# Kernel optimization log

Measured on AMD Instinct MI355X. Metric: run time of the kernel, lower is better.

## Reference

```python
import jax, jax.numpy as jnp
import numpy as np
import math

B, S, D, H = 2, 2048, 1024, 16
HD = D // H  # head_dims = 64


def setup_inputs() -> dict:
    key = jax.random.key(0)
    ks = jax.random.split(key, 8)
    sc = 1.0 / math.sqrt(D)
    return {
        "queries": jax.random.normal(ks[0], (B, S, D), jnp.float32),
        "keys":    jax.random.normal(ks[1], (B, S, D), jnp.float32),
        "values":  jax.random.normal(ks[2], (B, S, D), jnp.float32),
        # causal mask: 1 where attending allowed, 0 where blocked (masked_fill on ==0)
        "mask": jnp.tril(jnp.ones((S, S), jnp.int32)),
        "Wq": jax.random.normal(ks[3], (D, D), jnp.float32) * sc,
        "bq": jnp.zeros((D,), jnp.float32),
        "Wk": jax.random.normal(ks[4], (D, D), jnp.float32) * sc,
        "bk": jnp.zeros((D,), jnp.float32),
        "Wv": jax.random.normal(ks[5], (D, D), jnp.float32) * sc,
        "bv": jnp.zeros((D,), jnp.float32),
        "Wo": jax.random.normal(ks[6], (D, D), jnp.float32) * sc,
        "bo": jnp.zeros((D,), jnp.float32),
    }


def _split_heads(x):
    # (B, S, D) -> (B, H, S, HD)
    return x.reshape(B, S, H, HD).transpose(0, 2, 1, 3)


def reference(queries, keys, values, mask, Wq, bq, Wk, bk, Wv, bv, Wo, bo):
    q = queries @ Wq + bq
    k = keys @ Wk + bk
    # NOTE: faithful to source quirk — V is projected from the ALREADY-PROJECTED keys
    # (original: keys = self.W_keys(keys); values = self.W_values(keys))
    v = k @ Wv + bv
    q, k, v = _split_heads(q), _split_heads(k), _split_heads(v)
    # naive full NxN attention, as in the source
    scores = jnp.einsum("bhqd,bhkd->bhqk", q, k) / math.sqrt(HD)
    scores = jnp.where(mask == 0, jnp.float32(-1e9), scores)
    probs = jax.nn.softmax(scores, axis=-1)
    attn = jnp.einsum("bhqk,bhkd->bhqd", probs, v)
    attn = attn.transpose(0, 2, 1, 3).reshape(B, S, D)
    return attn @ Wo + bo
```

## Files before the change

kernel.cpp:

```cpp
#include <hip/hip_runtime.h>

typedef unsigned short u16;
typedef unsigned int u32;
typedef __bf16 bf16x8 __attribute__((ext_vector_type(8)));
typedef float f32x4 __attribute__((ext_vector_type(4)));
typedef float f32x16 __attribute__((ext_vector_type(16)));
typedef unsigned int u32x4v __attribute__((ext_vector_type(4)));

#define MFMA16(a, b, c) __builtin_amdgcn_mfma_f32_16x16x32_bf16(a, b, c, 0, 0, 0)
#define MFMA32(a, b, c) __builtin_amdgcn_mfma_f32_32x32x16_bf16(a, b, c, 0, 0, 0)

__device__ __forceinline__ void gload16(const void* g, void* l) {
  __builtin_amdgcn_global_load_lds((const __attribute__((address_space(1))) void*)g,
                                   (__attribute__((address_space(3))) void*)l, 16, 0, 0);
}

__device__ __forceinline__ u16 f2bf(float f) {
  u32 u = __builtin_bit_cast(u32, f);
  u += 0x7fffu + ((u >> 16) & 1u);
  return (u16)(u >> 16);
}
__device__ __forceinline__ u32 pack2(float a, float b) {
  u32 r;
  asm("v_cvt_pk_bf16_f32 %0, %1, %2" : "=v"(r) : "v"(a), "v"(b));
  return r;
}

__global__ __launch_bounds__(256) void cvt_kernel(const float* __restrict__ q,
                                                  const float* __restrict__ k,
                                                  u16* __restrict__ qb,
                                                  u16* __restrict__ kb) {
  const float* src = blockIdx.y ? k : q;
  u16* dst = blockIdx.y ? kb : qb;
  size_t i = (size_t)blockIdx.x * 256 + threadIdx.x;
  float4 v = ((const float4*)src)[i];
  uint2 o;
  o.x = pack2(v.x, v.y);
  o.y = pack2(v.z, v.w);
  ((uint2*)dst)[i] = o;
}

__global__ __launch_bounds__(256) void wtrans_kernel(const float* W0, const float* W1,
                                                     const float* W2, const float* W3,
                                                     u16* T0, u16* T1, u16* T2, u16* T3) {
  int z = blockIdx.z;
  const float* W = z == 0 ? W0 : z == 1 ? W1 : z == 2 ? W2 : W3;
  u16* T = z == 0 ? T0 : z == 1 ? T1 : z == 2 ? T2 : T3;
  __shared__ float tile[64][65];
  int tr = blockIdx.y * 64, tc = blockIdx.x * 64;
  int tid = threadIdx.x;
  int c4 = (tid & 15) * 4, r0 = tid >> 4;
#pragma unroll
  for (int i = 0; i < 4; i++) {
    int r = r0 + i * 16;
    float4 v = *(const float4*)(W + (size_t)(tr + r) * 1024 + tc + c4);
    tile[r][c4 + 0] = v.x; tile[r][c4 + 1] = v.y;
    tile[r][c4 + 2] = v.z; tile[r][c4 + 3] = v.w;
  }
  __syncthreads();
#pragma unroll
  for (int i = 0; i < 2; i++) {
    int c = tid + i * 256;
    int n = c >> 3, kg = c & 7;
    uint4 o;
    o.x = pack2(tile[kg * 8 + 0][n], tile[kg * 8 + 1][n]);
    o.y = pack2(tile[kg * 8 + 2][n], tile[kg * 8 + 3][n]);
    o.z = pack2(tile[kg * 8 + 4][n], tile[kg * 8 + 5][n]);
    o.w = pack2(tile[kg * 8 + 6][n], tile[kg * 8 + 7][n]);
    *(uint4*)(T + (size_t)(tc + n) * 1024 + tr + kg * 8) = o;
  }
}

template <int MODE>
__global__ __launch_bounds__(256) void gemm_kernel(
    const u16* A0, const u16* B0, const float* bias0, void* C0, float scale0,
    const u16* A1, const u16* B1, const float* bias1, void* C1, float scale1,
    int M, int N, int K) {
  const u16* A = A0; const u16* Bt = B0; const float* bias = bias0; void* Cout = C0;
  float scale = scale0;
  if (blockIdx.z) { A = A1; Bt = B1; bias = bias1; Cout = C1; scale = scale1; }

  __shared__ __attribute__((aligned(16))) char sAB[49152];
  const int tid = threadIdx.x, lane = tid & 63, w = tid >> 6;
  const int l15 = lane & 15, quad = lane >> 4;
  const int wm = (w >> 1) * 64, wn = (w & 1) * 32;
  const int m0 = blockIdx.y * 128, n0 = blockIdx.x * 64;

  const int lrow = lane >> 3, lcg = (lane & 7) ^ lrow;
  const u16* aP[4]; const u16* bP[2];
#pragma unroll
  for (int i = 0; i < 4; i++)
    aP[i] = A + (size_t)(m0 + w * 32 + i * 8 + lrow) * K + lcg * 8;
#pragma unroll
  for (int i = 0; i < 2; i++)
    bP[i] = Bt + (size_t)(n0 + w * 16 + i * 8 + lrow) * K + lcg * 8;

  int aoff[4], boff[2];
#pragma unroll
  for (int t = 0; t < 4; t++) {
    int ra = wm + t * 16 + l15;
    aoff[t] = ra * 128 + ((quad ^ (ra & 7)) * 16);
  }
#pragma unroll
  for (int t = 0; t < 2; t++) {
    int rb = wn + t * 16 + l15;
    boff[t] = 16384 + rb * 128 + ((quad ^ (rb & 7)) * 16);
  }

#pragma unroll
  for (int i = 0; i < 4; i++) { gload16(aP[i], sAB + w * 4096 + i * 1024); aP[i] += 64; }
#pragma unroll
  for (int i = 0; i < 2; i++) { gload16(bP[i], sAB + 16384 + w * 2048 + i * 1024); bP[i] += 64; }

  f32x4 acc[4][2] = {};
  int cur = 0;
  for (int k = 0; k < K; k += 64) {
    __syncthreads();
    if (k + 64 < K) {
      char* dst = sAB + (cur ^ 1) * 24576;
#pragma unroll
      for (int i = 0; i < 4; i++) { gload16(aP[i], dst + w * 4096 + i * 1024); aP[i] += 64; }
#pragma unroll
      for (int i = 0; i < 2; i++) { gload16(bP[i], dst + 16384 + w * 2048 + i * 1024); bP[i] += 64; }
    }
    const char* buf = sAB + cur * 24576;
#pragma unroll
    for (int kt = 0; kt < 2; kt++) {
      bf16x8 af[4], bfr[2];
#pragma unroll
      for (int t = 0; t < 4; t++) af[t] = *(const bf16x8*)(buf + (aoff[t] ^ (kt * 64)));
#pragma unroll
      for (int t = 0; t < 2; t++) bfr[t] = *(const bf16x8*)(buf + (boff[t] ^ (kt * 64)));
#pragma unroll
      for (int mt = 0; mt < 4; mt++)
#pragma unroll
        for (int nt = 0; nt < 2; nt++)
          acc[mt][nt] = MFMA16(af[mt], bfr[nt], acc[mt][nt]);
    }
    cur ^= 1;
  }

#pragma unroll
  for (int nt = 0; nt < 2; nt++) {
    int col = n0 + wn + nt * 16 + l15;
    float bv = bias[col];
#pragma unroll
    for (int mt = 0; mt < 4; mt++) {
      int row = m0 + wm + mt * 16 + quad * 4;
      if (MODE == 0) {
        u16* C = (u16*)Cout;
#pragma unroll
        for (int r = 0; r < 4; r++)
          C[(size_t)(row + r) * N + col] = f2bf((acc[mt][nt][r] + bv) * scale);
      } else if (MODE == 1) {
        u16* C = (u16*)Cout;
        int hh = col >> 6, hd = col & 63;
        int bb = row >> 11, s = row & 2047;
        uint2 o;
        o.x = pack2((acc[mt][nt][0] + bv) * scale, (acc[mt][nt][1] + bv) * scale);
        o.y = pack2((acc[mt][nt][2] + bv) * scale, (acc[mt][nt][3] + bv) * scale);
        *(uint2*)(C + ((size_t)((bb * 16 + hh) * 64 + hd) * 2048 + s)) = o;
      } else {
        float* C = (float*)Cout;
#pragma unroll
        for (int r = 0; r < 4; r++)
          C[(size_t)(row + r) * N + col] = (acc[mt][nt][r] + bv) * scale;
      }
    }
  }
}

__global__ __launch_bounds__(256, 2) void attn_kernel(const u16* __restrict__ qw,
                                                      const u16* __restrict__ kw,
                                                      const u16* __restrict__ vw,
                                                      u16* __restrict__ aout) {
  __shared__ __attribute__((aligned(16))) char sKV[4][16384];
  __shared__ float slq[4][64];
  char* sflat = (char*)sKV;
  const int bh = blockIdx.x, p = blockIdx.y;
  const int b = bh >> 4, h = bh & 15;
  const int tid = threadIdx.x, lane = tid & 63, w = tid >> 6;
  const int g = w & 1, kh = w >> 1;
  const int c = lane & 31, hi = lane >> 5;
  const int lrow = lane >> 3, lcg = (lane & 7) ^ lrow;
  const u16* kb0 = kw + (size_t)(b * 2048) * 1024 + h * 64;
  const u16* vb0 = vw + (size_t)bh * 64 * 2048;

  int koffK[4], koffV[2][2];
  {
    int krow = kh * 32 + c;
#pragma unroll
    for (int kt = 0; kt < 4; kt++)
      koffK[kt] = krow * 128 + (((kt * 2 + hi) ^ (krow & 7)) * 16);
#pragma unroll
    for (int m = 0; m < 2; m++) {
      int vrow = m * 32 + c;
#pragma unroll
      for (int kt2 = 0; kt2 < 2; kt2++)
        koffV[m][kt2] = 8192 + vrow * 128 + ((((kh * 2 + kt2) * 2 + hi) ^ (vrow & 7)) * 16);
    }
  }

  auto stage = [&](int j, int slot) {
    char* dst = sKV[slot];
#pragma unroll
    for (int i = 0; i < 2; i++) {
      int rr = w * 16 + i * 8 + lrow;
      gload16(kb0 + (size_t)(j * 64 + rr) * 1024 + lcg * 8, dst + w * 2048 + i * 1024);
      gload16(vb0 + (size_t)rr * 2048 + j * 64 + lcg * 8, dst + 8192 + w * 2048 + i * 1024);
    }
  };

  for (int phase = 0; phase < 2; ++phase) {
    const int t = phase ? (31 - p) : p;
    __syncthreads();

    bf16x8 qf[2][4];
#pragma unroll
    for (int qb2 = 0; qb2 < 2; qb2++) {
      const u16* qbase =
          qw + (size_t)(b * 2048 + t * 64 + qb2 * 32 + c) * 1024 + h * 64 + hi * 8;
#pragma unroll
      for (int kt = 0; kt < 4; kt++) qf[qb2][kt] = *(const bf16x8*)(qbase + kt * 16);
    }
    stage(0, 0);
    if (t >= 1) stage(1, 1);

    f32x16 o00 = {}, o01 = {}, o10 = {}, o11 = {};
    float ls0 = 0.f, ls1 = 0.f;
    const int R = (t + 2) >> 1;
    for (int r = 0; r < R; ++r) {
      __syncthreads();
      if (2 * r + 2 <= t) stage(2 * r + 2, (2 * r + 2) & 3);
      if (2 * r + 3 <= t) stage(2 * r + 3, (2 * r + 3) & 3);
      const int jg = 2 * r + g;
      if (jg <= t) {
        const char* buf = sKV[jg & 3];
        f32x16 S0 = {}, S1 = {};
        __builtin_amdgcn_s_setprio(1);
#pragma unroll
        for (int kt = 0; kt < 4; kt++) {
          bf16x8 kf = *(const bf16x8*)(buf + koffK[kt]);
          S0 = MFMA32(kf, qf[0][kt], S0);
          S1 = MFMA32(kf, qf[1][kt], S1);
        }
        __builtin_amdgcn_s_setprio(0);
        const bool diag = (jg == t);
        u32 pw0[8], pw1[8];
        auto epack = [&](const f32x16& S, int qc, u32* pw, float& ls) {
          float e[16];
#pragma unroll
          for (int rg = 0; rg < 16; rg++) {
            float ev = __builtin_amdgcn_exp2f(S[rg]);
            if (diag) {
              int row = kh * 32 + (rg & 3) + 8 * (rg >> 2) + 4 * hi;
              if (row > qc) ev = 0.f;
            }
            e[rg] = ev;
          }
          float s = 0.f;
#pragma unroll
          for (int rg = 0; rg < 16; rg += 4)
            s += (e[rg] + e[rg + 1]) + (e[rg + 2] + e[rg + 3]);
          ls += s;
#pragma unroll
          for (int i = 0; i < 8; i++) pw[i] = pack2(e[2 * i], e[2 * i + 1]);
        };
        epack(S0, c, pw0, ls0);
        epack(S1, 32 + c, pw1, ls1);
        __builtin_amdgcn_s_setprio(1);
#pragma unroll
        for (int kt2 = 0; kt2 < 2; kt2++) {
          const int bb = kt2 * 4;
          auto a0 = __builtin_amdgcn_permlane32_swap(pw0[bb + 0], pw0[bb + 2], false, false);
          auto a1 = __builtin_amdgcn_permlane32_swap(pw0[bb + 1], pw0[bb + 3], false, false);
          u32x4v pq0 = {a0[0], a1[0], a0[1], a1[1]};
          bf16x8 pf0 = __builtin_bit_cast(bf16x8, pq0);
          auto b0 = __builtin_amdgcn_permlane32_swap(pw1[bb + 0], pw1[bb + 2], false, false);
          auto b1 = __builtin_amdgcn_permlane32_swap(pw1[bb + 1], pw1[bb + 3], false, false);
          u32x4v pq1 = {b0[0], b1[0], b0[1], b1[1]};
          bf16x8 pf1 = __builtin_bit_cast(bf16x8, pq1);
          bf16x8 v0 = *(const bf16x8*)(buf + koffV[0][kt2]);
          bf16x8 v1 = *(const bf16x8*)(buf + koffV[1][kt2]);
          o00 = MFMA32(v0, pf0, o00);
          o10 = MFMA32(v1, pf0, o10);
          o01 = MFMA32(v0, pf1, o01);
          o11 = MFMA32(v1, pf1, o11);
        }
        __builtin_amdgcn_s_setprio(0);
      }
    }

    ls0 += __shfl_xor(ls0, 32, 64);
    ls1 += __shfl_xor(ls1, 32, 64);
    __syncthreads();
    {
      char* myr = sflat + w * 16384;
      auto putq = [&](int qid, const f32x16& v) {
#pragma unroll
        for (int ch = 0; ch < 4; ch++) {
          f32x4 x = {v[ch * 4 + 0], v[ch * 4 + 1], v[ch * 4 + 2], v[ch * 4 + 3]};
          *(f32x4*)(myr + (qid * 4 + ch) * 1024 + lane * 16) = x;
        }
      };
      putq(0, o00); putq(1, o01); putq(2, o10); putq(3, o11);
      slq[w][hi * 32 + c] = hi ? ls1 : ls0;
    }
    __syncthreads();
    {
      f32x16 acc = {};
#pragma unroll
      for (int wv = 0; wv < 4; wv++)
#pragma unroll
        for (int ch = 0; ch < 4; ch++) {
          f32x4 rr = *(const f32x4*)(sflat + wv * 16384 + (w * 4 + ch) * 1024 + lane * 16);
          acc[ch * 4 + 0] += rr[0]; acc[ch * 4 + 1] += rr[1];
          acc[ch * 4 + 2] += rr[2]; acc[ch * 4 + 3] += rr[3];
        }
      const int q = (w & 1) * 32 + c;
      float lt = ((slq[0][q] + slq[1][q]) + (slq[2][q] + slq[3][q]));
      float inv = 1.0f / lt;
      int token = b * 2048 + t * 64 + q;
      u16* outp = aout + (size_t)token * 1024 + h * 64 + (w >> 1) * 32;
#pragma unroll
      for (int i = 0; i < 4; i++) {
        uint2 ov;
        ov.x = pack2(acc[4 * i + 0] * inv, acc[4 * i + 1] * inv);
        ov.y = pack2(acc[4 * i + 2] * inv, acc[4 * i + 3] * inv);
        *(uint2*)(outp + i * 8 + hi * 4) = ov;
      }
    }
  }
}

extern "C" void kernel_launch(void* const* d_in, const int* in_sizes, int n_in,
                              void* d_out, int out_size, void* d_ws, size_t ws_size,
                              hipStream_t stream) {
  const float* queries = (const float*)d_in[0];
  const float* keys    = (const float*)d_in[1];
  const float* Wq = (const float*)d_in[4];
  const float* bq = (const float*)d_in[5];
  const float* Wk = (const float*)d_in[6];
  const float* bk = (const float*)d_in[7];
  const float* Wv = (const float*)d_in[8];
  const float* bv = (const float*)d_in[9];
  const float* Wo = (const float*)d_in[10];
  const float* bo = (const float*)d_in[11];

  char* ws = (char*)d_ws;
  u16* qb  = (u16*)(ws);
  u16* kb  = (u16*)(ws + (8u << 20));
  u16* qP  = (u16*)(ws + (16u << 20));
  u16* kP  = (u16*)(ws);
  u16* vP  = (u16*)(ws + (8u << 20));
  u16* WqT = (u16*)(ws + (24u << 20));
  u16* WkT = (u16*)(ws + (26u << 20));
  u16* WvT = (u16*)(ws + (28u << 20));
  u16* WoT = (u16*)(ws + (30u << 20));

  const float kscale = 1.4426950408889634f / 8.0f;

  cvt_kernel<<<dim3(4096, 2), 256, 0, stream>>>(queries, keys, qb, kb);
  wtrans_kernel<<<dim3(16, 16, 4), 256, 0, stream>>>(Wq, Wk, Wv, Wo, WqT, WkT, WvT, WoT);
  gemm_kernel<0><<<dim3(16, 32, 2), 256, 0, stream>>>(
      qb, WqT, bq, qP, kscale, kb, WkT, bk, kP, 1.0f, 4096, 1024, 1024);
  gemm_kernel<1><<<dim3(16, 32, 1), 256, 0, stream>>>(
      kP, WvT, bv, vP, 1.0f, kP, WvT, bv, vP, 1.0f, 4096, 1024, 1024);
  attn_kernel<<<dim3(32, 16), 256, 0, stream>>>(qP, kP, vP, qP);
  gemm_kernel<2><<<dim3(16, 32, 1), 256, 0, stream>>>(
      qP, WoT, bo, d_out, 1.0f, qP, WoT, bo, d_out, 1.0f, 4096, 1024, 1024);
}
```

Baseline: 215.4 us.

## Load GEMM B operand directly to registers, remap blocks, relax barrier wait

The projection GEMM no longer stages the B (weight) tile through LDS. Each lane loads its B fragments straight from global memory into registers, double-buffered one K step ahead. The block index is remapped so groups of 8 M-tiles share an N column for better L2 reuse of weights. The full __syncthreads is replaced by a partial vmcnt wait plus s_barrier so the register prefetch of B is not waited on. This trades LDS traffic and capacity for more VGPRs and uncoalesced per-lane global loads, and the hardcoded block mapping assumes a specific grid shape (32 M-tiles).

```diff
diff --git a/kernel.cpp b/kernel.cpp
--- a/kernel.cpp
+++ b/kernel.cpp
@@ -80,63 +80,78 @@
   float scale = scale0;
   if (blockIdx.z) { A = A1; Bt = B1; bias = bias1; Cout = C1; scale = scale1; }
 
-  __shared__ __attribute__((aligned(16))) char sAB[49152];
+  __shared__ __attribute__((aligned(16))) char sA[32768];
   const int tid = threadIdx.x, lane = tid & 63, w = tid >> 6;
   const int l15 = lane & 15, quad = lane >> 4;
   const int wm = (w >> 1) * 64, wn = (w & 1) * 32;
-  const int m0 = blockIdx.y * 128, n0 = blockIdx.x * 64;
+
+  const int bid = blockIdx.x + (int)(gridDim.x * blockIdx.y);
+  const int g8 = bid & 7, s = bid >> 3;
+  const int m0 = (g8 + (s & 3) * 8) * 128, n0 = (s >> 2) * 64;
 
   const int lrow = lane >> 3, lcg = (lane & 7) ^ lrow;
-  const u16* aP[4]; const u16* bP[2];
+  const u16* aP[4];
 #pragma unroll
   for (int i = 0; i < 4; i++)
     aP[i] = A + (size_t)(m0 + w * 32 + i * 8 + lrow) * K + lcg * 8;
-#pragma unroll
-  for (int i = 0; i < 2; i++)
-    bP[i] = Bt + (size_t)(n0 + w * 16 + i * 8 + lrow) * K + lcg * 8;
-
-  int aoff[4], boff[2];
+
+  const u16* bRow[2];
+#pragma unroll
+  for (int nt = 0; nt < 2; nt++)
+    bRow[nt] = Bt + (size_t)(n0 + wn + nt * 16 + l15) * K + quad * 8;
+
+  int aoff[4];
 #pragma unroll
   for (int t = 0; t < 4; t++) {
     int ra = wm + t * 16 + l15;
     aoff[t] = ra * 128 + ((quad ^ (ra & 7)) * 16);
   }
-#pragma unroll
-  for (int t = 0; t < 2; t++) {
-    int rb = wn + t * 16 + l15;
-    boff[t] = 16384 + rb * 128 + ((quad ^ (rb & 7)) * 16);
-  }
-
-#pragma unroll
-  for (int i = 0; i < 4; i++) { gload16(aP[i], sAB + w * 4096 + i * 1024); aP[i] += 64; }
-#pragma unroll
-  for (int i = 0; i < 2; i++) { gload16(bP[i], sAB + 16384 + w * 2048 + i * 1024); bP[i] += 64; }
+
+  auto stageA = [&](int buf) {
+    char* dst = sA + buf * 16384 + w * 4096;
+#pragma unroll
+    for (int i = 0; i < 4; i++) { gload16(aP[i], dst + i * 1024); aP[i] += 64; }
+  };
+
+  stageA(0);
+  bf16x8 bcur[2][2] = {}, bnxt[2][2] = {};
+#pragma unroll
+  for (int nt = 0; nt < 2; nt++)
+#pragma unroll
+    for (int kt = 0; kt < 2; kt++)
+      bcur[nt][kt] = *(const bf16x8*)(bRow[nt] + kt * 32);
 
   f32x4 acc[4][2] = {};
   int cur = 0;
   for (int k = 0; k < K; k += 64) {
-    __syncthreads();
+    asm volatile("s_waitcnt vmcnt(4)" ::: "memory");
+    __builtin_amdgcn_s_barrier();
+    asm volatile("" ::: "memory");
     if (k + 64 < K) {
-      char* dst = sAB + (cur ^ 1) * 24576;
-#pragma unroll
-      for (int i = 0; i < 4; i++) { gload16(aP[i], dst + w * 4096 + i * 1024); aP[i] += 64; }
-#pragma unroll
-      for (int i = 0; i < 2; i++) { gload16(bP[i], dst + 16384 + w * 2048 + i * 1024); bP[i] += 64; }
-    }
-    const char* buf = sAB + cur * 24576;
+      stageA(cur ^ 1);
+#pragma unroll
+      for (int nt = 0; nt < 2; nt++)
+#pragma unroll
+        for (int kt = 0; kt < 2; kt++)
+          bnxt[nt][kt] = *(const bf16x8*)(bRow[nt] + (k + 64) + kt * 32);
+    }
+    const char* buf = sA + cur * 16384;
 #pragma unroll
     for (int kt = 0; kt < 2; kt++) {
-      bf16x8 af[4], bfr[2];
+      bf16x8 af[4];
 #pragma unroll
       for (int t = 0; t < 4; t++) af[t] = *(const bf16x8*)(buf + (aoff[t] ^ (kt * 64)));
 #pragma unroll
-      for (int t = 0; t < 2; t++) bfr[t] = *(const bf16x8*)(buf + (boff[t] ^ (kt * 64)));
-#pragma unroll
       for (int mt = 0; mt < 4; mt++)
 #pragma unroll
         for (int nt = 0; nt < 2; nt++)
-          acc[mt][nt] = MFMA16(af[mt], bfr[nt], acc[mt][nt]);
-    }
+          acc[mt][nt] = MFMA16(af[mt], bcur[nt][kt], acc[mt][nt]);
+    }
+#pragma unroll
+    for (int nt = 0; nt < 2; nt++)
+#pragma unroll
+      for (int kt = 0; kt < 2; kt++)
+        bcur[nt][kt] = bnxt[nt][kt];
     cur ^= 1;
   }
 
@@ -155,11 +170,11 @@
       } else if (MODE == 1) {
         u16* C = (u16*)Cout;
         int hh = col >> 6, hd = col & 63;
-        int bb = row >> 11, s = row & 2047;
+        int bb = row >> 11, ss = row & 2047;
         uint2 o;
         o.x = pack2((acc[mt][nt][0] + bv) * scale, (acc[mt][nt][1] + bv) * scale);
         o.y = pack2((acc[mt][nt][2] + bv) * scale, (acc[mt][nt][3] + bv) * scale);
-        *(uint2*)(C + ((size_t)((bb * 16 + hh) * 64 + hd) * 2048 + s)) = o;
+        *(uint2*)(C + ((size_t)((bb * 16 + hh) * 64 + hd) * 2048 + ss)) = o;
       } else {
         float* C = (float*)Cout;
 #pragma unroll
@@ -258,11 +273,11 @@
             }
             e[rg] = ev;
           }
-          float s = 0.f;
+          float sAcc = 0.f;
 #pragma unroll
           for (int rg = 0; rg < 16; rg += 4)
-            s += (e[rg] + e[rg + 1]) + (e[rg + 2] + e[rg + 3]);
-          ls += s;
+            sAcc += (e[rg] + e[rg + 1]) + (e[rg + 2] + e[rg + 3]);
+          ls += sAcc;
 #pragma unroll
           for (int i = 0; i < 8; i++) pw[i] = pack2(e[2 * i], e[2 * i + 1]);
         };
```

Result: slower. 250.1 us (+16.1%).

## Load K/V fragments directly from global into registers, drop LDS staging

Applied to the files above, without the earlier changes.

Removes the LDS ring buffer and the global_load_lds staging of K/V tiles. Each wave now reads its own K and V MFMA fragments straight from global memory into registers, prefetching the next tile after finishing the current one, so the per-iteration block barriers go away. The cross-wave output reduction is split into two halves to shrink shared memory to 32KB, and the launch-bounds occupancy hint is dropped. The trade is uncoalesced, strided global reads with no reuse of K/V between waves, so the kernel leans on L2/cache bandwidth and latency hiding instead of LDS.

```diff
diff --git a/kernel.cpp b/kernel.cpp
--- a/kernel.cpp
+++ b/kernel.cpp
@@ -170,46 +170,23 @@
   }
 }
 
-__global__ __launch_bounds__(256, 2) void attn_kernel(const u16* __restrict__ qw,
-                                                      const u16* __restrict__ kw,
-                                                      const u16* __restrict__ vw,
-                                                      u16* __restrict__ aout) {
-  __shared__ __attribute__((aligned(16))) char sKV[4][16384];
+__global__ __launch_bounds__(256) void attn_kernel(const u16* __restrict__ qw,
+                                                   const u16* __restrict__ kw,
+                                                   const u16* __restrict__ vw,
+                                                   u16* __restrict__ aout) {
+  __shared__ __attribute__((aligned(16))) char sRed[32768];
   __shared__ float slq[4][64];
-  char* sflat = (char*)sKV;
   const int bh = blockIdx.x, p = blockIdx.y;
   const int b = bh >> 4, h = bh & 15;
   const int tid = threadIdx.x, lane = tid & 63, w = tid >> 6;
   const int g = w & 1, kh = w >> 1;
   const int c = lane & 31, hi = lane >> 5;
-  const int lrow = lane >> 3, lcg = (lane & 7) ^ lrow;
   const u16* kb0 = kw + (size_t)(b * 2048) * 1024 + h * 64;
   const u16* vb0 = vw + (size_t)bh * 64 * 2048;
 
-  int koffK[4], koffV[2][2];
-  {
-    int krow = kh * 32 + c;
-#pragma unroll
-    for (int kt = 0; kt < 4; kt++)
-      koffK[kt] = krow * 128 + (((kt * 2 + hi) ^ (krow & 7)) * 16);
-#pragma unroll
-    for (int m = 0; m < 2; m++) {
-      int vrow = m * 32 + c;
-#pragma unroll
-      for (int kt2 = 0; kt2 < 2; kt2++)
-        koffV[m][kt2] = 8192 + vrow * 128 + ((((kh * 2 + kt2) * 2 + hi) ^ (vrow & 7)) * 16);
-    }
-  }
-
-  auto stage = [&](int j, int slot) {
-    char* dst = sKV[slot];
-#pragma unroll
-    for (int i = 0; i < 2; i++) {
-      int rr = w * 16 + i * 8 + lrow;
-      gload16(kb0 + (size_t)(j * 64 + rr) * 1024 + lcg * 8, dst + w * 2048 + i * 1024);
-      gload16(vb0 + (size_t)rr * 2048 + j * 64 + lcg * 8, dst + 8192 + w * 2048 + i * 1024);
-    }
-  };
+  const u16* kbase = kb0 + (size_t)(kh * 32 + c) * 1024 + hi * 8;
+  const u16* vrow0 = vb0 + (size_t)(c) * 2048 + kh * 32 + hi * 8;
+  const u16* vrow1 = vb0 + (size_t)(32 + c) * 2048 + kh * 32 + hi * 8;
 
   for (int phase = 0; phase < 2; ++phase) {
     const int t = phase ? (31 - p) : p;
@@ -223,112 +200,133 @@
 #pragma unroll
       for (int kt = 0; kt < 4; kt++) qf[qb2][kt] = *(const bf16x8*)(qbase + kt * 16);
     }
-    stage(0, 0);
-    if (t >= 1) stage(1, 1);
 
     f32x16 o00 = {}, o01 = {}, o10 = {}, o11 = {};
     float ls0 = 0.f, ls1 = 0.f;
-    const int R = (t + 2) >> 1;
-    for (int r = 0; r < R; ++r) {
-      __syncthreads();
-      if (2 * r + 2 <= t) stage(2 * r + 2, (2 * r + 2) & 3);
-      if (2 * r + 3 <= t) stage(2 * r + 3, (2 * r + 3) & 3);
-      const int jg = 2 * r + g;
-      if (jg <= t) {
-        const char* buf = sKV[jg & 3];
-        f32x16 S0 = {}, S1 = {};
-        __builtin_amdgcn_s_setprio(1);
-#pragma unroll
-        for (int kt = 0; kt < 4; kt++) {
-          bf16x8 kf = *(const bf16x8*)(buf + koffK[kt]);
-          S0 = MFMA32(kf, qf[0][kt], S0);
-          S1 = MFMA32(kf, qf[1][kt], S1);
+
+    bf16x8 kf[4], vf[2][2];
+    auto loadKV = [&](int j) {
+      const u16* kp = kbase + (size_t)j * 65536;
+#pragma unroll
+      for (int kt = 0; kt < 4; kt++) kf[kt] = *(const bf16x8*)(kp + kt * 16);
+#pragma unroll
+      for (int kt2 = 0; kt2 < 2; kt2++) {
+        vf[0][kt2] = *(const bf16x8*)(vrow0 + j * 64 + kt2 * 16);
+        vf[1][kt2] = *(const bf16x8*)(vrow1 + j * 64 + kt2 * 16);
+      }
+    };
+    if (g <= t) loadKV(g);
+    for (int j = g; j <= t; j += 2) {
+      f32x16 S0 = {}, S1 = {};
+      __builtin_amdgcn_s_setprio(1);
+#pragma unroll
+      for (int kt = 0; kt < 4; kt++) {
+        S0 = MFMA32(kf[kt], qf[0][kt], S0);
+        S1 = MFMA32(kf[kt], qf[1][kt], S1);
+      }
+      __builtin_amdgcn_s_setprio(0);
+      const bool diag = (j == t);
+      u32 pw0[8], pw1[8];
+      auto epack = [&](const f32x16& S, int qc, u32* pw, float& ls) {
+        float e[16];
+#pragma unroll
+        for (int rg = 0; rg < 16; rg++) {
+          float ev = __builtin_amdgcn_exp2f(S[rg]);
+          if (diag) {
+            int row = kh * 32 + (rg & 3) + 8 * (rg >> 2) + 4 * hi;
+            if (row > qc) ev = 0.f;
+          }
+          e[rg] = ev;
         }
-        __builtin_amdgcn_s_setprio(0);
-        const bool diag = (jg == t);
-        u32 pw0[8], pw1[8];
-        auto epack = [&](const f32x16& S, int qc, u32* pw, float& ls) {
-          float e[16];
-#pragma unroll
-          for (int rg = 0; rg < 16; rg++) {
-            float ev = __builtin_amdgcn_exp2f(S[rg]);
-            if (diag) {
-              int row = kh * 32 + (rg & 3) + 8 * (rg >> 2) + 4 * hi;
-              if (row > qc) ev = 0.f;
-            }
-            e[rg] = ev;
-          }
-          float s = 0.f;
-#pragma unroll
-          for (int rg = 0; rg < 16; rg += 4)
-            s += (e[rg] + e[rg + 1]) + (e[rg + 2] + e[rg + 3]);
-          ls += s;
-#pragma unroll
-          for (int i = 0; i < 8; i++) pw[i] = pack2(e[2 * i], e[2 * i + 1]);
-        };
-        epack(S0, c, pw0, ls0);
-        epack(S1, 32 + c, pw1, ls1);
-        __builtin_amdgcn_s_setprio(1);
-#pragma unroll
-        for (int kt2 = 0; kt2 < 2; kt2++) {
-          const int bb = kt2 * 4;
-          auto a0 = __builtin_amdgcn_permlane32_swap(pw0[bb + 0], pw0[bb + 2], false, false);
-          auto a1 = __builtin_amdgcn_permlane32_swap(pw0[bb + 1], pw0[bb + 3], false, false);
-          u32x4v pq0 = {a0[0], a1[0], a0[1], a1[1]};
-          bf16x8 pf0 = __builtin_bit_cast(bf16x8, pq0);
-          auto b0 = __builtin_amdgcn_permlane32_swap(pw1[bb + 0], pw1[bb + 2], false, false);
-          auto b1 = __builtin_amdgcn_permlane32_swap(pw1[bb + 1], pw1[bb + 3], false, false);
-          u32x4v pq1 = {b0[0], b1[0], b0[1], b1[1]};
-          bf16x8 pf1 = __builtin_bit_cast(bf16x8, pq1);
-          bf16x8 v0 = *(const bf16x8*)(buf + koffV[0][kt2]);
-          bf16x8 v1 = *(const bf16x8*)(buf + koffV[1][kt2]);
-          o00 = MFMA32(v0, pf0, o00);
-          o10 = MFMA32(v1, pf0, o10);
-          o01 = MFMA32(v0, pf1, o01);
-          o11 = MFMA32(v1, pf1, o11);
-        }
-        __builtin_amdgcn_s_setprio(0);
-      }
+        float sAcc = 0.f;
+#pragma unroll
+        for (int rg = 0; rg < 16; rg += 4)
+          sAcc += (e[rg] + e[rg + 1]) + (e[rg + 2] + e[rg + 3]);
+        ls += sAcc;
+#pragma unroll
+        for (int i = 0; i < 8; i++) pw[i] = pack2(e[2 * i], e[2 * i + 1]);
+      };
+      epack(S0, c, pw0, ls0);
+      epack(S1, 32 + c, pw1, ls1);
+      __builtin_amdgcn_s_setprio(1);
+#pragma unroll
+      for (int kt2 = 0; kt2 < 2; kt2++) {
+        const int bb = kt2 * 4;
+        auto a0 = __builtin_amdgcn_permlane32_swap(pw0[bb + 0], pw0[bb + 2], false, false);
+        auto a1 = __builtin_amdgcn_permlane32_swap(pw0[bb + 1], pw0[bb + 3], false, false);
+        u32x4v pq0 = {a0[0], a1[0], a0[1], a1[1]};
+        bf16x8 pf0 = __builtin_bit_cast(bf16x8, pq0);
+        auto b0 = __builtin_amdgcn_permlane32_swap(pw1[bb + 0], pw1[bb + 2], false, false);
+        auto b1 = __builtin_amdgcn_permlane32_swap(pw1[bb + 1], pw1[bb + 3], false, false);
+        u32x4v pq1 = {b0[0], b1[0], b0[1], b1[1]};
+        bf16x8 pf1 = __builtin_bit_cast(bf16x8, pq1);
+        o00 = MFMA32(vf[0][kt2], pf0, o00);
+        o10 = MFMA32(vf[1][kt2], pf0, o10);
+        o01 = MFMA32(vf[0][kt2], pf1, o01);
+        o11 = MFMA32(vf[1][kt2], pf1, o11);
+      }
+      __builtin_amdgcn_s_setprio(0);
+      if (j + 2 <= t) loadKV(j + 2);
     }
 
     ls0 += __shfl_xor(ls0, 32, 64);
     ls1 += __shfl_xor(ls1, 32, 64);
-    __syncthreads();
+    slq[w][hi * 32 + c] = hi ? ls1 : ls0;
     {
-      char* myr = sflat + w * 16384;
-      auto putq = [&](int qid, const f32x16& v) {
-#pragma unroll
-        for (int ch = 0; ch < 4; ch++) {
-          f32x4 x = {v[ch * 4 + 0], v[ch * 4 + 1], v[ch * 4 + 2], v[ch * 4 + 3]};
-          *(f32x4*)(myr + (qid * 4 + ch) * 1024 + lane * 16) = x;
-        }
-      };
-      putq(0, o00); putq(1, o01); putq(2, o10); putq(3, o11);
-      slq[w][hi * 32 + c] = hi ? ls1 : ls0;
+      char* myr = sRed + w * 8192;
+#pragma unroll
+      for (int ch = 0; ch < 4; ch++) {
+        f32x4 x0 = {o00[ch * 4 + 0], o00[ch * 4 + 1], o00[ch * 4 + 2], o00[ch * 4 + 3]};
+        *(f32x4*)(myr + ch * 1024 + lane * 16) = x0;
+        f32x4 x1 = {o01[ch * 4 + 0], o01[ch * 4 + 1], o01[ch * 4 + 2], o01[ch * 4 + 3]};
+        *(f32x4*)(myr + 4096 + ch * 1024 + lane * 16) = x1;
+      }
+    }
+    __syncthreads();
+    const int qh = w & 1, cp = (w >> 1) * 2;
+    const int q = qh * 32 + c;
+    const float lt = (slq[0][q] + slq[1][q]) + (slq[2][q] + slq[3][q]);
+    const float inv = 1.0f / lt;
+    u16* outp = aout + (size_t)(b * 2048 + t * 64 + q) * 1024 + h * 64;
+#pragma unroll
+    for (int cc = 0; cc < 2; cc++) {
+      const int ch = cp + cc;
+      f32x4 s = {};
+#pragma unroll
+      for (int wv = 0; wv < 4; wv++) {
+        f32x4 rr = *(const f32x4*)(sRed + wv * 8192 + qh * 4096 + ch * 1024 + lane * 16);
+        s[0] += rr[0]; s[1] += rr[1]; s[2] += rr[2]; s[3] += rr[3];
+      }
+      uint2 ov;
+      ov.x = pack2(s[0] * inv, s[1] * inv);
+      ov.y = pack2(s[2] * inv, s[3] * inv);
+      *(uint2*)(outp + ch * 8 + hi * 4) = ov;
     }
     __syncthreads();
     {
-      f32x16 acc = {};
-#pragma unroll
-      for (int wv = 0; wv < 4; wv++)
-#pragma unroll
-        for (int ch = 0; ch < 4; ch++) {
-          f32x4 rr = *(const f32x4*)(sflat + wv * 16384 + (w * 4 + ch) * 1024 + lane * 16);
-          acc[ch * 4 + 0] += rr[0]; acc[ch * 4 + 1] += rr[1];
-          acc[ch * 4 + 2] += rr[2]; acc[ch * 4 + 3] += rr[3];
-        }
-      const int q = (w & 1) * 32 + c;
-      float lt = ((slq[0][q] + slq[1][q]) + (slq[2][q] + slq[3][q]));
-      float inv = 1.0f / lt;
-      int token = b * 2048 + t * 64 + q;
-      u16* outp = aout + (size_t)token * 1024 + h * 64 + (w >> 1) * 32;
-#pragma unroll
-      for (int i = 0; i < 4; i++) {
-        uint2 ov;
-        ov.x = pack2(acc[4 * i + 0] * inv, acc[4 * i + 1] * inv);
-        ov.y = pack2(acc[4 * i + 2] * inv, acc[4 * i + 3] * inv);
-        *(uint2*)(outp + i * 8 + hi * 4) = ov;
-      }
+      char* myr = sRed + w * 8192;
+#pragma unroll
+      for (int ch = 0; ch < 4; ch++) {
+        f32x4 x0 = {o10[ch * 4 + 0], o10[ch * 4 + 1], o10[ch * 4 + 2], o10[ch * 4 + 3]};
+        *(f32x4*)(myr + ch * 1024 + lane * 16) = x0;
+        f32x4 x1 = {o11[ch * 4 + 0], o11[ch * 4 + 1], o11[ch * 4 + 2], o11[ch * 4 + 3]};
+        *(f32x4*)(myr + 4096 + ch * 1024 + lane * 16) = x1;
+      }
+    }
+    __syncthreads();
+#pragma unroll
+    for (int cc = 0; cc < 2; cc++) {
+      const int ch = cp + cc;
+      f32x4 s = {};
+#pragma unroll
+      for (int wv = 0; wv < 4; wv++) {
+        f32x4 rr = *(const f32x4*)(sRed + wv * 8192 + qh * 4096 + ch * 1024 + lane * 16);
+        s[0] += rr[0]; s[1] += rr[1]; s[2] += rr[2]; s[3] += rr[3];
+      }
+      uint2 ov;
+      ov.x = pack2(s[0] * inv, s[1] * inv);
+      ov.y = pack2(s[2] * inv, s[3] * inv);
+      *(uint2*)(outp + 32 + ch * 8 + hi * 4) = ov;
     }
   }
 }
```

New measurement: 228.1 us. 1.06x slower.

## Triple-buffer GEMM LDS staging with explicit vmcnt waits and single barrier

Applied to the files above, without the earlier changes.

Changes the projection GEMM kernel from double buffering to a three-stage LDS ring. Loads are issued two tiles ahead, and each iteration waits with an explicit vmcnt(6) and one raw s_barrier instead of a full __syncthreads. This is meant to hide more global-load latency and trim synchronization. The cost is LDS rising from 48KB to 72KB per block, which may reduce occupancy. A variable rename in the attention kernel is cosmetic.

```diff
diff --git a/kernel.cpp b/kernel.cpp
--- a/kernel.cpp
+++ b/kernel.cpp
@@ -80,7 +80,7 @@
   float scale = scale0;
   if (blockIdx.z) { A = A1; Bt = B1; bias = bias1; Cout = C1; scale = scale1; }
 
-  __shared__ __attribute__((aligned(16))) char sAB[49152];
+  __shared__ __attribute__((aligned(16))) char sAB[73728];
   const int tid = threadIdx.x, lane = tid & 63, w = tid >> 6;
   const int l15 = lane & 15, quad = lane >> 4;
   const int wm = (w >> 1) * 64, wn = (w & 1) * 32;
@@ -107,23 +107,24 @@
     boff[t] = 16384 + rb * 128 + ((quad ^ (rb & 7)) * 16);
   }
 
-#pragma unroll
-  for (int i = 0; i < 4; i++) { gload16(aP[i], sAB + w * 4096 + i * 1024); aP[i] += 64; }
-#pragma unroll
-  for (int i = 0; i < 2; i++) { gload16(bP[i], sAB + 16384 + w * 2048 + i * 1024); bP[i] += 64; }
+  auto stage = [&](char* dst) {
+#pragma unroll
+    for (int i = 0; i < 4; i++) { gload16(aP[i], dst + w * 4096 + i * 1024); aP[i] += 64; }
+#pragma unroll
+    for (int i = 0; i < 2; i++) { gload16(bP[i], dst + 16384 + w * 2048 + i * 1024); bP[i] += 64; }
+  };
+
+  const int NIT = K >> 6;
+  stage(sAB);
+  stage(sAB + 24576);
 
   f32x4 acc[4][2] = {};
-  int cur = 0;
-  for (int k = 0; k < K; k += 64) {
-    __syncthreads();
-    if (k + 64 < K) {
-      char* dst = sAB + (cur ^ 1) * 24576;
-#pragma unroll
-      for (int i = 0; i < 4; i++) { gload16(aP[i], dst + w * 4096 + i * 1024); aP[i] += 64; }
-#pragma unroll
-      for (int i = 0; i < 2; i++) { gload16(bP[i], dst + 16384 + w * 2048 + i * 1024); bP[i] += 64; }
-    }
-    const char* buf = sAB + cur * 24576;
+  for (int i = 0; i < NIT - 1; ++i) {
+    asm volatile("s_waitcnt vmcnt(6)" ::: "memory");
+    __builtin_amdgcn_s_barrier();
+    asm volatile("" ::: "memory");
+    if (i + 2 < NIT) stage(sAB + ((i + 2) % 3) * 24576);
+    const char* buf = sAB + (i % 3) * 24576;
 #pragma unroll
     for (int kt = 0; kt < 2; kt++) {
       bf16x8 af[4], bfr[2];
@@ -137,7 +138,25 @@
         for (int nt = 0; nt < 2; nt++)
           acc[mt][nt] = MFMA16(af[mt], bfr[nt], acc[mt][nt]);
     }
-    cur ^= 1;
+  }
+  {
+    asm volatile("s_waitcnt vmcnt(0)" ::: "memory");
+    __builtin_amdgcn_s_barrier();
+    asm volatile("" ::: "memory");
+    const char* buf = sAB + ((NIT - 1) % 3) * 24576;
+#pragma unroll
+    for (int kt = 0; kt < 2; kt++) {
+      bf16x8 af[4], bfr[2];
+#pragma unroll
+      for (int t = 0; t < 4; t++) af[t] = *(const bf16x8*)(buf + (aoff[t] ^ (kt * 64)));
+#pragma unroll
+      for (int t = 0; t < 2; t++) bfr[t] = *(const bf16x8*)(buf + (boff[t] ^ (kt * 64)));
+#pragma unroll
+      for (int mt = 0; mt < 4; mt++)
+#pragma unroll
+        for (int nt = 0; nt < 2; nt++)
+          acc[mt][nt] = MFMA16(af[mt], bfr[nt], acc[mt][nt]);
+    }
   }
 
 #pragma unroll
@@ -258,11 +277,11 @@
             }
             e[rg] = ev;
           }
-          float s = 0.f;
+          float sAcc = 0.f;
 #pragma unroll
           for (int rg = 0; rg < 16; rg += 4)
-            s += (e[rg] + e[rg + 1]) + (e[rg + 2] + e[rg + 3]);
-          ls += s;
+            sAcc += (e[rg] + e[rg + 1]) + (e[rg + 2] + e[rg + 3]);
+          ls += sAcc;
 #pragma unroll
           for (int i = 0; i < 8; i++) pw[i] = pack2(e[2 * i], e[2 * i + 1]);
         };
```

Result: slower. 224.7 us (+4.3%).
